# Optimization experiments

Measured on AMD Instinct MI355X. Metric: run time of the kernel, lower is better.

Reference implementation:

```python
import jax, jax.numpy as jnp
import numpy as np

ENS, S_DIM, A_DIM, R_DIM, HID, LAYER_NUM = 7, 30, 8, 1, 200, 5
N_HID_LAYERS = LAYER_NUM - 2  # hidden->hidden Linear+Swish blocks


def swish(x):
    return x * jax.nn.sigmoid(x)


def setup_inputs() -> dict:
    key = jax.random.key(0)
    ks = jax.random.split(key, 14)
    N = 32768
    out_dim = S_DIM + R_DIM
    s = jax.random.normal(ks[0], (N, ENS, S_DIM), dtype=jnp.float32)
    a = jax.random.normal(ks[1], (N, ENS, A_DIM), dtype=jnp.float32)
    sc = 0.05
    W1 = jax.random.normal(ks[2], (ENS, S_DIM + A_DIM, HID), dtype=jnp.float32) * sc
    b1 = jax.random.normal(ks[3], (ENS, HID), dtype=jnp.float32) * sc
    Wh = jax.random.normal(ks[4], (N_HID_LAYERS, ENS, HID, HID), dtype=jnp.float32) * sc
    bh = jax.random.normal(ks[5], (N_HID_LAYERS, ENS, HID), dtype=jnp.float32) * sc
    Wmu = jax.random.normal(ks[6], (ENS, HID, out_dim), dtype=jnp.float32) * sc
    bmu = jax.random.normal(ks[7], (ENS, out_dim), dtype=jnp.float32) * sc
    Wsig = jax.random.normal(ks[8], (ENS, HID, out_dim), dtype=jnp.float32) * sc
    bsig = jax.random.normal(ks[9], (ENS, out_dim), dtype=jnp.float32) * sc
    max_lv_s = jnp.ones((1, S_DIM), dtype=jnp.float32) / 2.0
    min_lv_s = jnp.ones((1, S_DIM), dtype=jnp.float32) * -10.0
    max_lv_r = jnp.ones((1, R_DIM), dtype=jnp.float32) / 2.0
    min_lv_r = jnp.ones((1, R_DIM), dtype=jnp.float32) * -10.0
    return {"s": s, "a": a, "W1": W1, "b1": b1, "Wh": Wh, "bh": bh,
            "Wmu": Wmu, "bmu": bmu, "Wsig": Wsig, "bsig": bsig,
            "max_lv_s": max_lv_s, "min_lv_s": min_lv_s,
            "max_lv_r": max_lv_r, "min_lv_r": min_lv_r}


def reference(s, a, W1, b1, Wh, bh, Wmu, bmu, Wsig, bsig,
              max_lv_s, min_lv_s, max_lv_r, min_lv_r):
    # x: [N, E, s+a]; per-ensemble-member weights batched along E
    x = jnp.concatenate([s, a], axis=-1)
    h = swish(jnp.einsum('ned,edh->neh', x, W1) + b1)
    for i in range(Wh.shape[0]):
        h = swish(jnp.einsum('neh,ehk->nek', h, Wh[i]) + bh[i])
    mu = jnp.einsum('neh,eho->neo', h, Wmu) + bmu      # [N, E, s+r]
    sigma = jnp.einsum('neh,eho->neo', h, Wsig) + bsig  # raw logvar/2
    ds_mu, r_mu = mu[..., :S_DIM], mu[..., S_DIM:]
    ds_sg, r_sg = sigma[..., :S_DIM], sigma[..., S_DIM:]
    # soft clamping of log-variance, then exp
    ds_sg = (max_lv_s - jax.nn.softplus(max_lv_s - 2.0 * ds_sg)) / 2.0
    ds_sg = (min_lv_s + jax.nn.softplus(2.0 * ds_sg - min_lv_s)) / 2.0
    ds_sg = jnp.exp(ds_sg)
    r_sg = (max_lv_r - jax.nn.softplus(max_lv_r - 2.0 * r_sg)) / 2.0
    r_sg = (min_lv_r + jax.nn.softplus(2.0 * r_sg - min_lv_r)) / 2.0
    r_sg = jnp.exp(r_sg)
    return ((ds_mu, ds_sg), (r_mu, r_sg))
```

## Files before the change

kernel.cpp:

```cpp
#include <hip/hip_runtime.h>

#define ENS 7
#define SDIM 30
#define ADIM 8
#define DIN 38
#define HID 200
#define DOUT 31
#define NHL 3
#define HS 232
#define MT 64

typedef __bf16 bf16x8 __attribute__((ext_vector_type(8)));
typedef float f32x4 __attribute__((ext_vector_type(4)));

#define U_L1 13312
#define U_H 46592
#define OFF_HD2 (U_L1 + NHL * U_H)
#define PER_E (OFF_HD2 + 14336)
#define WS_TOTAL (ENS * PER_E)

__device__ __forceinline__ unsigned short f2bf(float f) {
    unsigned u = __float_as_uint(f);
    u += 0x7fffu + ((u >> 16) & 1u);
    return (unsigned short)(u >> 16);
}

__device__ __forceinline__ float softplusf(float x) {
    return fmaxf(x, 0.f) + __logf(1.f + __expf(-fabsf(x)));
}

__global__ void prep_kernel(const float* __restrict__ W1, const float* __restrict__ Wh,
                            const float* __restrict__ Wmu, const float* __restrict__ Wsig,
                            unsigned short* __restrict__ ws) {
    int idx = blockIdx.x * 256 + threadIdx.x;
    if (idx >= WS_TOTAL) return;
    int e = idx / PER_E, r = idx % PER_E;
    int j = r & 7, lane = (r >> 3) & 63;
    int l16 = lane & 15, q = lane >> 4;
    float v = 0.f;
    if (r < U_L1) {
        int fi = r >> 9;
        int ct = fi >> 1, st = fi & 1;
        int k = st * 32 + q * 8 + j, n = ct * 16 + l16;
        if (k < DIN && n < HID) v = W1[(e * DIN + k) * HID + n];
    } else if (r < OFF_HD2) {
        int rh = r - U_L1;
        int l = rh / U_H, r2 = rh % U_H;
        int fi = r2 >> 9;
        int ct = fi / 7, st = fi % 7;
        int k = st * 32 + q * 8 + j, n = ct * 16 + l16;
        if (k < HID && n < HID) v = Wh[((l * ENS + e) * HID + (long)k) * HID + n];
    } else {
        int r2 = r - OFF_HD2;
        int fi = r2 >> 9;
        int ct = fi / 7, st = fi % 7;
        int k = st * 32 + q * 8 + j, n = ct * 16 + l16;
        if (k < HID) {
            if (n < DOUT) v = Wmu[(e * HID + k) * DOUT + n];
            else if (n >= 32 && n < 32 + DOUT) v = Wsig[(e * HID + k) * DOUT + (n - 32)];
        }
    }
    ws[idx] = f2bf(v);
}

template<int S, int NT>
__device__ __forceinline__ void runLayer(const unsigned short* __restrict__ gB,
                                         const unsigned short* hA,
                                         int wv, int l16, int quad,
                                         f32x4 acc[4][4]) {
#pragma unroll
    for (int r = 0; r < 4; r++)
#pragma unroll
        for (int j = 0; j < 4; j++) acc[r][j] = (f32x4){0.f, 0.f, 0.f, 0.f};

    const unsigned short* fp = gB + (quad * 16 + l16) * 8;
    bf16x8 bcur[4], bnxt[4];
#pragma unroll
    for (int j = 0; j < 4; j++) {
        int ct = wv + 4 * j;
        if (ct < NT) bcur[j] = *((const bf16x8*)(fp + (ct * S) * 512));
    }
#pragma unroll
    for (int st = 0; st < S; ++st) {
        if (st + 1 < S) {
#pragma unroll
            for (int j = 0; j < 4; j++) {
                int ct = wv + 4 * j;
                if (ct < NT) bnxt[j] = *((const bf16x8*)(fp + (ct * S + st + 1) * 512));
            }
        }
        bf16x8 af[4];
#pragma unroll
        for (int r = 0; r < 4; r++)
            af[r] = *((const bf16x8*)(hA + (r * 16 + l16) * HS + st * 32 + quad * 8));
#pragma unroll
        for (int j = 0; j < 4; j++) {
            int ct = wv + 4 * j;
            if (ct < NT) {
#pragma unroll
                for (int r = 0; r < 4; r++)
                    acc[r][j] = __builtin_amdgcn_mfma_f32_16x16x32_bf16(af[r], bcur[j], acc[r][j], 0, 0, 0);
            }
        }
#pragma unroll
        for (int j = 0; j < 4; j++) bcur[j] = bnxt[j];
    }
}

__launch_bounds__(256, 3)
__global__ void ens_mlp_kernel(const float* __restrict__ s, const float* __restrict__ a,
                               const float* __restrict__ b1, const float* __restrict__ bh,
                               const float* __restrict__ bmu, const float* __restrict__ bsig,
                               const float* __restrict__ maxs, const float* __restrict__ mins,
                               const float* __restrict__ maxr, const float* __restrict__ minr,
                               const unsigned short* __restrict__ ws,
                               float* __restrict__ out, int N) {
    __shared__ unsigned short hA[MT * HS];

    const int tid = threadIdx.x;
    const int wv = tid >> 6, lane = tid & 63;
    const int quad = lane >> 4, l16 = lane & 15;
    const int bid = blockIdx.x;
    const int e = bid % ENS, n0 = (bid / ENS) * MT;

    for (int i = tid; i < MT * HS / 8; i += 256) ((uint4*)hA)[i] = make_uint4(0, 0, 0, 0);
    __syncthreads();

    for (int i = tid; i < MT * DIN; i += 256) {
        int m = i / DIN, c = i % DIN;
        long g = n0 + m;
        float v = (c < SDIM) ? s[(g * ENS + e) * SDIM + c]
                             : a[(g * ENS + e) * ADIM + (c - SDIM)];
        hA[m * HS + c] = f2bf(v);
    }
    __syncthreads();

    f32x4 acc[4][4];

    auto epiH = [&](const float* bias) {
#pragma unroll
        for (int j = 0; j < 4; j++) {
            int ct = wv + 4 * j;
            if (ct < 13) {
                int col = ct * 16 + l16;
                float bc = (col < HID) ? bias[col] : 0.f;
#pragma unroll
                for (int r = 0; r < 4; r++)
#pragma unroll
                    for (int i = 0; i < 4; i++) {
                        float v = acc[r][j][i] + bc;
                        float sw = v * __builtin_amdgcn_rcpf(1.f + __expf(-v));
                        hA[(r * 16 + quad * 4 + i) * HS + col] = f2bf(sw);
                    }
            }
        }
    };

    const unsigned short* we = ws + e * PER_E;

    runLayer<2, 13>(we, hA, wv, l16, quad, acc);
    __syncthreads();
    epiH(b1 + e * HID);
    __syncthreads();
#pragma unroll
    for (int l = 0; l < NHL; l++) {
        runLayer<7, 13>(we + U_L1 + l * U_H, hA, wv, l16, quad, acc);
        __syncthreads();
        epiH(bh + (l * ENS + e) * HID);
        __syncthreads();
    }
    runLayer<7, 4>(we + OFF_HD2, hA, wv, l16, quad, acc);
    __syncthreads();

    float* scr = (float*)hA;
    {
        int col = wv * 16 + l16;
        float bc = 0.f;
        if (col < DOUT) bc = bmu[e * DOUT + col];
        else if (col >= 32 && col < 32 + DOUT) bc = bsig[e * DOUT + (col - 32)];
#pragma unroll
        for (int r = 0; r < 4; r++)
#pragma unroll
            for (int i = 0; i < 4; i++)
                scr[(r * 16 + quad * 4 + i) * 64 + col] = acc[r][0][i] + bc;
    }
    __syncthreads();

    const long off1 = (long)N * ENS * SDIM;
    const long off2 = 2 * off1;
    const long off3 = off2 + (long)N * ENS;

    for (int i = tid; i < MT * DOUT; i += 256) {
        int m = i / DOUT, c = i % DOUT;
        long g = n0 + m;
        float v = scr[m * 64 + c];
        if (c < SDIM) out[(g * ENS + e) * SDIM + c] = v;
        else out[off2 + g * ENS + e] = v;
    }
    for (int i = tid; i < MT * DOUT; i += 256) {
        int m = i / DOUT, c = i % DOUT;
        long g = n0 + m;
        float v = scr[m * 64 + 32 + c];
        float mx = (c < SDIM) ? maxs[c] : maxr[0];
        float mn = (c < SDIM) ? mins[c] : minr[0];
        v = 0.5f * (mx - softplusf(mx - 2.f * v));
        v = 0.5f * (mn + softplusf(2.f * v - mn));
        v = __expf(v);
        if (c < SDIM) out[off1 + (g * ENS + e) * SDIM + c] = v;
        else out[off3 + g * ENS + e] = v;
    }
}

extern "C" void kernel_launch(void* const* d_in, const int* in_sizes, int n_in,
                              void* d_out, int out_size, void* d_ws, size_t ws_size,
                              hipStream_t stream) {
    const float* s    = (const float*)d_in[0];
    const float* a    = (const float*)d_in[1];
    const float* W1   = (const float*)d_in[2];
    const float* b1   = (const float*)d_in[3];
    const float* Wh   = (const float*)d_in[4];
    const float* bh   = (const float*)d_in[5];
    const float* Wmu  = (const float*)d_in[6];
    const float* bmu  = (const float*)d_in[7];
    const float* Wsig = (const float*)d_in[8];
    const float* bsig = (const float*)d_in[9];
    const float* maxs = (const float*)d_in[10];
    const float* mins = (const float*)d_in[11];
    const float* maxr = (const float*)d_in[12];
    const float* minr = (const float*)d_in[13];
    float* out = (float*)d_out;
    unsigned short* ws = (unsigned short*)d_ws;

    int N = in_sizes[0] / (ENS * SDIM);

    int prepBlocks = (WS_TOTAL + 255) / 256;
    prep_kernel<<<prepBlocks, 256, 0, stream>>>(W1, Wh, Wmu, Wsig, ws);

    int mainBlocks = (N / MT) * ENS;
    ens_mlp_kernel<<<mainBlocks, 256, 0, stream>>>(s, a, b1, bh, bmu, bsig,
                                                   maxs, mins, maxr, minr, ws, out, N);
}
```

Measured before the change: 272.6 us.

## Swap MFMA operands to transpose accumulators and vectorize epilogue stores

Swaps the A and B operands of the MFMA so that each lane's four accumulator values lie along consecutive output columns rather than consecutive rows. The swish epilogue can then load a float4 bias and write packed bf16 pairs with one 8-byte LDS store per row, instead of four scalar 2-byte stores. The final layer's results are written to global memory directly from registers, removing the LDS scratch round trip and two barriers. The input staging loop is also restructured so each thread handles one row. Global output stores become less coalesced, since each lane writes four consecutive floats of a different row.

```diff
diff --git a/kernel.cpp b/kernel.cpp
--- a/kernel.cpp
+++ b/kernel.cpp
@@ -1,4 +1,5 @@
 #include <hip/hip_runtime.h>
+#include <hip/hip_bf16.h>
 
 #define ENS 7
 #define SDIM 30
@@ -23,6 +24,11 @@
     unsigned u = __float_as_uint(f);
     u += 0x7fffu + ((u >> 16) & 1u);
     return (unsigned short)(u >> 16);
+}
+
+__device__ __forceinline__ unsigned pk2(float a, float b) {
+    __hip_bfloat162 h = __float22bfloat162_rn(make_float2(a, b));
+    return *reinterpret_cast<unsigned*>(&h);
 }
 
 __device__ __forceinline__ float softplusf(float x) {
@@ -66,14 +72,14 @@
 template<int S, int NT>
 __device__ __forceinline__ void runLayer(const unsigned short* __restrict__ gB,
                                          const unsigned short* hA,
-                                         int wv, int l16, int quad,
+                                         int wv, int lane, int l16, int quad,
                                          f32x4 acc[4][4]) {
 #pragma unroll
     for (int r = 0; r < 4; r++)
 #pragma unroll
         for (int j = 0; j < 4; j++) acc[r][j] = (f32x4){0.f, 0.f, 0.f, 0.f};
 
-    const unsigned short* fp = gB + (quad * 16 + l16) * 8;
+    const unsigned short* fp = gB + lane * 8;
     bf16x8 bcur[4], bnxt[4];
 #pragma unroll
     for (int j = 0; j < 4; j++) {
@@ -99,7 +105,7 @@
             if (ct < NT) {
 #pragma unroll
                 for (int r = 0; r < 4; r++)
-                    acc[r][j] = __builtin_amdgcn_mfma_f32_16x16x32_bf16(af[r], bcur[j], acc[r][j], 0, 0, 0);
+                    acc[r][j] = __builtin_amdgcn_mfma_f32_16x16x32_bf16(bcur[j], af[r], acc[r][j], 0, 0, 0);
             }
         }
 #pragma unroll
@@ -126,12 +132,19 @@
     for (int i = tid; i < MT * HS / 8; i += 256) ((uint4*)hA)[i] = make_uint4(0, 0, 0, 0);
     __syncthreads();
 
-    for (int i = tid; i < MT * DIN; i += 256) {
-        int m = i / DIN, c = i % DIN;
+    {
+        int m = tid & 63, cg = tid >> 6;
         long g = n0 + m;
-        float v = (c < SDIM) ? s[(g * ENS + e) * SDIM + c]
-                             : a[(g * ENS + e) * ADIM + (c - SDIM)];
-        hA[m * HS + c] = f2bf(v);
+        const float* srow = s + (g * ENS + e) * SDIM;
+        const float* arow = a + (g * ENS + e) * ADIM;
+#pragma unroll
+        for (int k = 0; k < 10; k++) {
+            int c = cg * 10 + k;
+            if (c < DIN) {
+                float v = (c < SDIM) ? srow[c] : arow[c - SDIM];
+                hA[m * HS + c] = f2bf(v);
+            }
+        }
     }
     __syncthreads();
 
@@ -142,72 +155,77 @@
         for (int j = 0; j < 4; j++) {
             int ct = wv + 4 * j;
             if (ct < 13) {
-                int col = ct * 16 + l16;
-                float bc = (col < HID) ? bias[col] : 0.f;
-#pragma unroll
-                for (int r = 0; r < 4; r++)
-#pragma unroll
-                    for (int i = 0; i < 4; i++) {
-                        float v = acc[r][j][i] + bc;
-                        float sw = v * __builtin_amdgcn_rcpf(1.f + __expf(-v));
-                        hA[(r * 16 + quad * 4 + i) * HS + col] = f2bf(sw);
-                    }
+                int col = ct * 16 + quad * 4;
+                float4 bc4 = make_float4(0.f, 0.f, 0.f, 0.f);
+                if (col < HID) bc4 = *((const float4*)(bias + col));
+#pragma unroll
+                for (int r = 0; r < 4; r++) {
+                    int row = r * 16 + l16;
+                    float v0 = acc[r][j][0] + bc4.x, v1 = acc[r][j][1] + bc4.y;
+                    float v2 = acc[r][j][2] + bc4.z, v3 = acc[r][j][3] + bc4.w;
+                    v0 *= __builtin_amdgcn_rcpf(1.f + __expf(-v0));
+                    v1 *= __builtin_amdgcn_rcpf(1.f + __expf(-v1));
+                    v2 *= __builtin_amdgcn_rcpf(1.f + __expf(-v2));
+                    v3 *= __builtin_amdgcn_rcpf(1.f + __expf(-v3));
+                    *((uint2*)(hA + row * HS + col)) = make_uint2(pk2(v0, v1), pk2(v2, v3));
+                }
             }
         }
     };
 
     const unsigned short* we = ws + e * PER_E;
 
-    runLayer<2, 13>(we, hA, wv, l16, quad, acc);
+    runLayer<2, 13>(we, hA, wv, lane, l16, quad, acc);
     __syncthreads();
     epiH(b1 + e * HID);
     __syncthreads();
 #pragma unroll
     for (int l = 0; l < NHL; l++) {
-        runLayer<7, 13>(we + U_L1 + l * U_H, hA, wv, l16, quad, acc);
+        runLayer<7, 13>(we + U_L1 + l * U_H, hA, wv, lane, l16, quad, acc);
         __syncthreads();
         epiH(bh + (l * ENS + e) * HID);
         __syncthreads();
     }
-    runLayer<7, 4>(we + OFF_HD2, hA, wv, l16, quad, acc);
-    __syncthreads();
-
-    float* scr = (float*)hA;
-    {
-        int col = wv * 16 + l16;
-        float bc = 0.f;
-        if (col < DOUT) bc = bmu[e * DOUT + col];
-        else if (col >= 32 && col < 32 + DOUT) bc = bsig[e * DOUT + (col - 32)];
-#pragma unroll
-        for (int r = 0; r < 4; r++)
-#pragma unroll
-            for (int i = 0; i < 4; i++)
-                scr[(r * 16 + quad * 4 + i) * 64 + col] = acc[r][0][i] + bc;
-    }
-    __syncthreads();
+    runLayer<7, 4>(we + OFF_HD2, hA, wv, lane, l16, quad, acc);
 
     const long off1 = (long)N * ENS * SDIM;
     const long off2 = 2 * off1;
     const long off3 = off2 + (long)N * ENS;
-
-    for (int i = tid; i < MT * DOUT; i += 256) {
-        int m = i / DOUT, c = i % DOUT;
-        long g = n0 + m;
-        float v = scr[m * 64 + c];
-        if (c < SDIM) out[(g * ENS + e) * SDIM + c] = v;
-        else out[off2 + g * ENS + e] = v;
-    }
-    for (int i = tid; i < MT * DOUT; i += 256) {
-        int m = i / DOUT, c = i % DOUT;
-        long g = n0 + m;
-        float v = scr[m * 64 + 32 + c];
-        float mx = (c < SDIM) ? maxs[c] : maxr[0];
-        float mn = (c < SDIM) ? mins[c] : minr[0];
-        v = 0.5f * (mx - softplusf(mx - 2.f * v));
-        v = 0.5f * (mn + softplusf(2.f * v - mn));
-        v = __expf(v);
-        if (c < SDIM) out[off1 + (g * ENS + e) * SDIM + c] = v;
-        else out[off3 + g * ENS + e] = v;
+    {
+        const bool isSig = (wv >= 2);
+        const int c0 = (wv & 1) * 16 + quad * 4;
+        float bias_i[4], mx_i[4], mn_i[4];
+#pragma unroll
+        for (int i = 0; i < 4; i++) {
+            int c = c0 + i;
+            bias_i[i] = (c < DOUT) ? (isSig ? bsig : bmu)[e * DOUT + c] : 0.f;
+            if (isSig) {
+                mx_i[i] = (c < SDIM) ? maxs[c] : maxr[0];
+                mn_i[i] = (c < SDIM) ? mins[c] : minr[0];
+            }
+        }
+#pragma unroll
+        for (int r = 0; r < 4; r++) {
+            long g = n0 + r * 16 + l16;
+            long rowbase = (g * ENS + e) * SDIM;
+#pragma unroll
+            for (int i = 0; i < 4; i++) {
+                int c = c0 + i;
+                if (c < DOUT) {
+                    float v = acc[r][0][i] + bias_i[i];
+                    if (!isSig) {
+                        if (c < SDIM) out[rowbase + c] = v;
+                        else out[off2 + g * ENS + e] = v;
+                    } else {
+                        v = 0.5f * (mx_i[i] - softplusf(mx_i[i] - 2.f * v));
+                        v = 0.5f * (mn_i[i] + softplusf(2.f * v - mn_i[i]));
+                        v = __expf(v);
+                        if (c < SDIM) out[off1 + rowbase + c] = v;
+                        else out[off3 + g * ENS + e] = v;
+                    }
+                }
+            }
+        }
     }
 }
 
```

Result: faster. 264.3 us (-3.0%).
